# Performance work log

Measured on AMD Instinct MI355X. Metric: run time of the kernel, lower is better.

The kernel has to match this reference:

```python
import jax, jax.numpy as jnp
import numpy as np

TEMPERATURES = (0.02, 0.05, 0.2)
NORMALIZE_FEATURES = True
NORMALIZE_DRIFT = True
EPS = 1e-8


def _sqdist(a, b):
    # ||a_i - b_j||^2 via expansion; clamp tiny negatives from fp error
    aa = jnp.sum(a * a, axis=1)[:, None]
    bb = jnp.sum(b * b, axis=1)[None, :]
    return jnp.maximum(aa + bb - 2.0 * (a @ b.T), 0.0)


def compute_drifting_field(x, y_pos, y_neg, temperatures):
    """Multi-scale RBF-kernel drifting field.

    V(x) = mean_tau [ softmax_j(-d(x,y_pos_j)/tau) @ y_pos
                    - softmax_k(-d(x,y_neg_k)/tau) @ y_neg ]
    (the attraction/repulsion (y - x) terms: the -x cancels between pos and neg)
    Returns (V, raw_drift_norm, lambda_V).
    """
    D = x.shape[1]
    if NORMALIZE_FEATURES:
        # scale-invariant distances: global RMS of the reference samples
        ref = jnp.concatenate([y_pos, y_neg], axis=0)
        scale = jnp.sqrt(jnp.mean(ref * ref) + EPS)
    else:
        scale = jnp.asarray(1.0, x.dtype)
    xs, yp, yn = x / scale, y_pos / scale, y_neg / scale

    d_pos = _sqdist(xs, yp)  # [N, N_pos]
    d_neg = _sqdist(xs, yn)  # [N, N_neg]

    V = jnp.zeros_like(xs)
    for tau in temperatures:
        w_pos = jax.nn.softmax(-d_pos / tau, axis=1)
        w_neg = jax.nn.softmax(-d_neg / tau, axis=1)
        V = V + (w_pos @ yp - w_neg @ yn)
    V = (V / len(temperatures)) * scale  # back to original feature scale

    raw_drift_norm = jnp.mean(jnp.sum(V * V, axis=1))  # E[||V_raw||^2]
    lambda_V = jnp.sqrt(raw_drift_norm / D + EPS)
    if NORMALIZE_DRIFT:
        V = V / lambda_V
    return V, raw_drift_norm, lambda_V


def reference(x, y_pos, y_neg):
    V, raw_drift_norm, lambda_V = compute_drifting_field(x, y_pos, y_neg, TEMPERATURES)
    x_target = jax.lax.stop_gradient(x + V)
    loss_per_sample = jnp.mean((x - x_target) ** 2, axis=1)
    loss = jnp.mean(loss_per_sample)  # reduction='mean'
    drift_norm = jnp.mean(jnp.sum(V * V, axis=1))
    # per-temperature logging: original redundantly recomputes the full field
    per_temp = jnp.stack([
        compute_drifting_field(x, y_pos, y_neg, (tau,))[1] for tau in TEMPERATURES
    ])
    return loss, drift_norm, raw_drift_norm, lambda_V, per_temp, jax.lax.stop_gradient(V)


def setup_inputs() -> dict:
    key = jax.random.key(0)
    k1, k2, k3 = jax.random.split(key, 3)
    N, D = 4096, 256
    return {
        "x": jax.random.normal(k1, (N, D), dtype=jnp.float32),
        "y_pos": jax.random.normal(k2, (N, D), dtype=jnp.float32),
        "y_neg": jax.random.normal(k3, (N, D), dtype=jnp.float32),
    }
```

## Files before the change

kernel.cpp:

```cpp
#include <hip/hip_runtime.h>

#define NPTS 4096
#define DIM  256
#define TIL  64
#define WCAND 32

typedef unsigned short u16;
typedef unsigned long long u64;
typedef __attribute__((ext_vector_type(8))) short bf16x8;
typedef __attribute__((ext_vector_type(4))) float f32x4;
typedef __attribute__((ext_vector_type(4))) unsigned short u16x4;

__device__ __forceinline__ float exp2fast(float x) {
  float r;
  asm("v_exp_f32 %0, %1" : "=v"(r) : "v"(x));
  return r;
}

__device__ __forceinline__ void gload_lds16(const void* g, void* l) {
  __builtin_amdgcn_global_load_lds((const __attribute__((address_space(1))) void*)g,
                                   (__attribute__((address_space(3))) void*)l, 16, 0, 0);
}

__device__ __forceinline__ float blk_sum(float v, float* sh) {
  #pragma unroll
  for (int off = 32; off; off >>= 1) v += __shfl_down(v, off);
  int lane = threadIdx.x & 63, w = threadIdx.x >> 6;
  __syncthreads();
  if (lane == 0) sh[w] = v;
  __syncthreads();
  return sh[0] + sh[1] + sh[2] + sh[3];
}

__device__ __forceinline__ float block_scalesq(
    const float* __restrict__ bbp, const float* __restrict__ bbn, float* red, int tid) {
  float s = 0.f;
  #pragma unroll
  for (int q = 0; q < 4; ++q) {
    f32x4 a = *reinterpret_cast<const f32x4*>(bbp + (q * 256 + tid) * 4);
    f32x4 b = *reinterpret_cast<const f32x4*>(bbn + (q * 256 + tid) * 4);
    s += a[0] + a[1] + a[2] + a[3] + b[0] + b[1] + b[2] + b[3];
  }
  float tot = blk_sum(s, red);
  return tot * (1.0f / (2.0f * NPTS * DIM)) + 1e-8f;
}

__global__ __launch_bounds__(256) void split3_kernel(
    const float* __restrict__ x, const float* __restrict__ yp, const float* __restrict__ yn,
    u16* __restrict__ xb, u16* __restrict__ ypb, u16* __restrict__ ynb,
    float* __restrict__ bbp, float* __restrict__ bbn)
{
  const float* src; u16* dst; float* bb;
  if      (blockIdx.y == 0) { src = x;  dst = xb;  bb = nullptr; }
  else if (blockIdx.y == 1) { src = yp; dst = ypb; bb = bbp; }
  else                      { src = yn; dst = ynb; bb = bbn; }

  int lane = threadIdx.x & 63;
  int wave = threadIdx.x >> 6;
  int row  = blockIdx.x * 4 + wave;
  const float4 v = *reinterpret_cast<const float4*>(src + (size_t)row * DIM + lane * 4);
  float xs[4] = {v.x, v.y, v.z, v.w};
  u16x4 h;
  float ss = 0.f;
  #pragma unroll
  for (int e = 0; e < 4; ++e) {
    unsigned b = __float_as_uint(xs[e]);
    h[e] = (u16)((b + 0x7fffu + ((b >> 16) & 1u)) >> 16);
    ss += xs[e] * xs[e];
  }
  *reinterpret_cast<u16x4*>(dst + (size_t)row * DIM + lane * 4) = h;
  if (bb) {
    #pragma unroll
    for (int off = 32; off; off >>= 1) ss += __shfl_down(ss, off);
    if (lane == 0) bb[row] = ss;
  }
}

__global__ __launch_bounds__(256, 3) void gemm_kernel(
    const u16* __restrict__ Xb, const u16* __restrict__ Ypb, const u16* __restrict__ Ynb,
    const float* __restrict__ bbp, const float* __restrict__ bbn,
    float* __restrict__ M, u64* __restrict__ Kmask)
{
  __shared__ u16 Ah[3][128 * 32];
  __shared__ u16 Bh[3][128 * 32];
  __shared__ float red[4];

  const int tid  = threadIdx.x;

  const unsigned lid = blockIdx.x + (blockIdx.y << 5) + (blockIdx.z << 10);
  const unsigned swz = (lid & 7) * 256 + (lid >> 3);
  const int bx = swz & 31, by = (swz >> 5) & 31, side = (int)(swz >> 10);

  const u16* Yb = side ? Ynb : Ypb;
  const float* bbv = side ? bbn : bbp;

  const float scalesq = block_scalesq(bbp, bbn, red, tid);

  const int lane = tid & 63;
  const int wave = tid >> 6;
  const int wm = wave >> 1, wn = wave & 1;
  const int l15 = lane & 15, lhi = lane >> 4;

  const int rf = bx * 128;
  const int cf = by * 128;
  const int til = by * 2 + wn;

  const int r0  = tid >> 2;
  const int r1  = (tid + 256) >> 2;
  const int pc  = tid & 3;
  const int gc0 = pc ^ (r0 & 3);
  const int gc1 = pc ^ (r1 & 3);

  f32x4 acc[4][4] = {};

#define STAGE(KS, BUF)                                                                    \
  do {                                                                                    \
    int ko_ = (KS) * 32;                                                                  \
    gload_lds16(Xb + (size_t)(rf + r0) * DIM + ko_ + gc0 * 8, Ah[BUF] + r0 * 32 + pc * 8);\
    gload_lds16(Yb + (size_t)(cf + r0) * DIM + ko_ + gc0 * 8, Bh[BUF] + r0 * 32 + pc * 8);\
    gload_lds16(Xb + (size_t)(rf + r1) * DIM + ko_ + gc1 * 8, Ah[BUF] + r1 * 32 + pc * 8);\
    gload_lds16(Yb + (size_t)(cf + r1) * DIM + ko_ + gc1 * 8, Bh[BUF] + r1 * 32 + pc * 8);\
  } while (0)

  STAGE(0, 0);
  STAGE(1, 1);

  #pragma unroll 1
  for (int ks = 0; ks < 8; ++ks) {
    const int cur = ks % 3;
    if (ks < 7) asm volatile("s_waitcnt vmcnt(4)" ::: "memory");
    else        asm volatile("s_waitcnt vmcnt(0)" ::: "memory");
    __builtin_amdgcn_s_barrier();
    __builtin_amdgcn_sched_barrier(0);

    if (ks < 6) STAGE(ks + 2, (ks + 2) % 3);

    bf16x8 a[4], b[4];
    #pragma unroll
    for (int mi = 0; mi < 4; ++mi) {
      int R = wm * 64 + mi * 16 + l15;
      a[mi] = *reinterpret_cast<const bf16x8*>(Ah[cur] + R * 32 + ((lhi ^ (R & 3)) * 8));
    }
    #pragma unroll
    for (int ni = 0; ni < 4; ++ni) {
      int R = wn * 64 + ni * 16 + l15;
      b[ni] = *reinterpret_cast<const bf16x8*>(Bh[cur] + R * 32 + ((lhi ^ (R & 3)) * 8));
    }
    #pragma unroll
    for (int mi = 0; mi < 4; ++mi)
      #pragma unroll
      for (int ni = 0; ni < 4; ++ni)
        acc[mi][ni] = __builtin_amdgcn_mfma_f32_16x16x32_bf16(a[mi], b[ni], acc[mi][ni], 0, 0, 0);
  }
#undef STAGE

  const float thrP = 30.0f * scalesq * 0.2f + 2.5f * scalesq + 0.5f;

  float bbc[4];
  #pragma unroll
  for (int ni = 0; ni < 4; ++ni) bbc[ni] = bbv[cf + wn * 64 + ni * 16 + l15];

  #pragma unroll
  for (int mi = 0; mi < 4; ++mi)
    #pragma unroll
    for (int r = 0; r < 4; ++r) {
      float uv[4];
      float mx = -3.0e38f;
      #pragma unroll
      for (int ni = 0; ni < 4; ++ni) {
        uv[ni] = 2.0f * acc[mi][ni][r] - bbc[ni];
        mx = fmaxf(mx, uv[ni]);
      }
      #pragma unroll
      for (int off = 1; off < 16; off <<= 1) mx = fmaxf(mx, __shfl_xor(mx, off));
      const float cut = mx - thrP;

      u64 bal[4];
      #pragma unroll
      for (int ni = 0; ni < 4; ++ni) bal[ni] = __ballot(uv[ni] > cut);

      u64 mask = 0;
      #pragma unroll
      for (int ni = 0; ni < 4; ++ni)
        mask |= ((bal[ni] >> (lhi * 16)) & 0xFFFFull) << (ni * 16);

      const int rowG = rf + wm * 64 + mi * 16 + lhi * 4 + r;
      if (l15 == 0) {
        Kmask[((size_t)side * TIL + til) * NPTS + rowG] = mask;
        M[((size_t)side * NPTS + rowG) * TIL + til] = mx;
      }
    }
}

__global__ __launch_bounds__(256) void row_kernel(
    const float* __restrict__ M, const u64* __restrict__ Kmask,
    const float* __restrict__ bbp, const float* __restrict__ bbn,
    const float* __restrict__ x,
    const float* __restrict__ ypos, const float* __restrict__ yneg,
    float* __restrict__ parts, float* __restrict__ Vout)
{
  __shared__ unsigned cl[4][WCAND];
  __shared__ float red[4];

  const int tid  = threadIdx.x;
  const int lane = tid & 63;
  const int w    = tid >> 6;
  const int row  = blockIdx.x * 4 + w;

  const float scalesq = block_scalesq(bbp, bbn, red, tid);
  const float L2E = 1.4426950408889634f;
  const float c0 = L2E / (scalesq * 0.02f);
  const float c1 = L2E / (scalesq * 0.05f);
  const float c2 = L2E / (scalesq * 0.2f);
  const float thrP = 30.0f * scalesq * 0.2f + 2.5f * scalesq + 0.5f;

  const f32x4 xv = *reinterpret_cast<const f32x4*>(x + (size_t)row * DIM + lane * 4);

  f32x4 V0 = {0,0,0,0}, V1 = {0,0,0,0}, V2 = {0,0,0,0};

  for (int side = 0; side < 2; ++side) {
    const float* bb = side ? bbn : bbp;
    const float* y  = side ? yneg : ypos;
    const float sgn = side ? -1.f : 1.f;

    float Mv = M[((size_t)side * NPTS + row) * TIL + lane];
    float g = Mv;
    #pragma unroll
    for (int off = 32; off; off >>= 1) g = fmaxf(g, __shfl_xor(g, off));
    const float cut = g - thrP;

    u64 mm = __ballot(Mv > cut);
    int nc = 0;
    while (mm) {
      int t = __ffsll((long long)mm) - 1;
      mm &= mm - 1;
      u64 mask = Kmask[((size_t)side * TIL + t) * NPTS + row];
      bool keep = (mask >> lane) & 1ull;
      int rank = __popcll(mask & ((1ull << lane) - 1ull));
      if (keep && nc + rank < WCAND) cl[w][nc + rank] = t * 64 + lane;
      nc += __popcll(mask);
    }
    nc = nc < WCAND ? nc : WCAND;

    float me = -3.0e38f, p0 = 0.f, p1 = 0.f, p2 = 0.f;
    f32x4 A0 = {0,0,0,0}, A1 = {0,0,0,0}, A2 = {0,0,0,0};
    for (int bs = 0; bs < nc; bs += 8) {
      const int rem = nc - bs;
      int jq[8];
      f32x4 yv[8];
      float dq[8], uq[8];
      #pragma unroll
      for (int q = 0; q < 8; ++q) {
        int idx = (q < rem) ? bs + q : bs;
        jq[q] = (int)cl[w][idx];
        yv[q] = *reinterpret_cast<const f32x4*>(y + (size_t)jq[q] * DIM + lane * 4);
      }
      #pragma unroll
      for (int q = 0; q < 8; ++q)
        dq[q] = xv[0]*yv[q][0] + xv[1]*yv[q][1] + xv[2]*yv[q][2] + xv[3]*yv[q][3];
      #pragma unroll
      for (int off = 32; off; off >>= 1)
        #pragma unroll
        for (int q = 0; q < 8; ++q) dq[q] += __shfl_xor(dq[q], off);
      #pragma unroll
      for (int q = 0; q < 8; ++q)
        uq[q] = (q < rem) ? 2.0f * dq[q] - bb[jq[q]] : -3.0e38f;

      float cm = uq[0];
      #pragma unroll
      for (int q = 1; q < 8; ++q) cm = fmaxf(cm, uq[q]);
      float nm = fmaxf(me, cm);
      float s0 = exp2fast((me - nm) * c0);
      float s1 = exp2fast((me - nm) * c1);
      float s2 = exp2fast((me - nm) * c2);
      p0 *= s0; p1 *= s1; p2 *= s2;
      A0 *= s0; A1 *= s1; A2 *= s2;
      #pragma unroll
      for (int q = 0; q < 8; ++q) {
        float du = uq[q] - nm;
        float e0 = exp2fast(du * c0);
        float e1 = exp2fast(du * c1);
        float e2 = exp2fast(du * c2);
        p0 += e0; p1 += e1; p2 += e2;
        A0 += e0 * yv[q]; A1 += e1 * yv[q]; A2 += e2 * yv[q];
      }
      me = nm;
    }
    V0 += (sgn / p0) * A0;
    V1 += (sgn / p1) * A1;
    V2 += (sgn / p2) * A2;
  }

  f32x4 vr = (V0 + V1 + V2) * (1.0f / 3.0f);
  *reinterpret_cast<f32x4*>(Vout + (size_t)row * DIM + lane * 4) = vr;

  float s0 = V0[0]*V0[0] + V0[1]*V0[1] + V0[2]*V0[2] + V0[3]*V0[3];
  float s1 = V1[0]*V1[0] + V1[1]*V1[1] + V1[2]*V1[2] + V1[3]*V1[3];
  float s2 = V2[0]*V2[0] + V2[1]*V2[1] + V2[2]*V2[2] + V2[3]*V2[3];
  float sr = vr[0]*vr[0] + vr[1]*vr[1] + vr[2]*vr[2] + vr[3]*vr[3];
  #pragma unroll
  for (int off = 32; off; off >>= 1) {
    s0 += __shfl_xor(s0, off);
    s1 += __shfl_xor(s1, off);
    s2 += __shfl_xor(s2, off);
    sr += __shfl_xor(sr, off);
  }
  if (lane == 0) {
    parts[row]            = sr;
    parts[NPTS + row]     = s0;
    parts[2 * NPTS + row] = s1;
    parts[3 * NPTS + row] = s2;
  }
}

__global__ __launch_bounds__(256) void final_kernel(
    const float* __restrict__ parts, float* __restrict__ out)
{
  __shared__ float red[4];
  const int tid = threadIdx.x;

  float s = 0.f;
  for (int k = tid; k < NPTS; k += 256) s += parts[k];
  float raw = blk_sum(s, red) * (1.0f / NPTS);
  float lam2 = raw * (1.0f / DIM) + 1e-8f;
  float lam  = sqrtf(lam2);
  float inv  = 1.0f / lam;

  int idx = blockIdx.x * 256 + tid;
  out[7 + idx] *= inv;

  if (blockIdx.x == 0) {
    #pragma unroll
    for (int a = 1; a <= 3; ++a) {
      float t = 0.f;
      for (int k = tid; k < NPTS; k += 256) t += parts[a * NPTS + k];
      t = blk_sum(t, red);
      if (tid == 0) out[3 + a] = t * (1.0f / NPTS);
    }
    if (tid == 0) {
      float drift = raw / lam2;
      out[0] = drift * (1.0f / DIM);
      out[1] = drift;
      out[2] = raw;
      out[3] = lam;
    }
  }
}

extern "C" void kernel_launch(void* const* d_in, const int* in_sizes, int n_in,
                              void* d_out, int out_size, void* d_ws, size_t ws_size,
                              hipStream_t stream)
{
  (void)in_sizes; (void)n_in; (void)out_size; (void)ws_size;
  const float* x    = (const float*)d_in[0];
  const float* ypos = (const float*)d_in[1];
  const float* yneg = (const float*)d_in[2];
  float* out = (float*)d_out;
  char* ws = (char*)d_ws;

  float* bbp   = (float*)ws;
  float* bbn   = (float*)(ws + 16384);
  float* parts = (float*)(ws + 32768);
  float* M     = (float*)(ws + 98304);
  u64*   Kmask = (u64*)(ws + 98304 + 2097152);
  u16* xb  = (u16*)(ws + 98304 + 2097152 + 4194304);
  u16* ypb = xb + (size_t)NPTS * DIM;
  u16* ynb = xb + 2 * (size_t)NPTS * DIM;

  split3_kernel<<<dim3(NPTS / 4, 3), 256, 0, stream>>>(x, ypos, yneg, xb, ypb, ynb, bbp, bbn);
  gemm_kernel<<<dim3(32, 32, 2), 256, 0, stream>>>(xb, ypb, ynb, bbp, bbn, M, Kmask);
  row_kernel<<<NPTS / 4, 256, 0, stream>>>(M, Kmask, bbp, bbn, x, ypos, yneg,
                                           parts, out + 7);
  final_kernel<<<NPTS, 256, 0, stream>>>(parts, out);
}
```

Before: 83.35 us.

## Fuse pos/neg GEMMs per block to share X tile loads

Each GEMM block now computes both the positive and negative distance tiles for the same X rows, loading the X tile once and reusing it for two B tiles. This halves the grid, doubles the accumulators, and drops from triple to double buffering with a full vmcnt(0) wait each step. The LDS swizzle pattern also changes. The cost is higher register pressure, which may hurt occupancy at launch_bounds(256,3), and a less deep load pipeline.

New measurement: 118.6 us. 42.3% more time.

```diff
diff --git a/kernel.cpp b/kernel.cpp
--- a/kernel.cpp
+++ b/kernel.cpp
@@ -81,18 +81,16 @@
     const float* __restrict__ bbp, const float* __restrict__ bbn,
     float* __restrict__ M, u64* __restrict__ Kmask)
 {
-  __shared__ u16 Ah[3][128 * 32];
-  __shared__ u16 Bh[3][128 * 32];
+  __shared__ u16 Ah[2][128 * 32];
+  __shared__ u16 Bp[2][128 * 32];
+  __shared__ u16 Bn[2][128 * 32];
   __shared__ float red[4];
 
   const int tid  = threadIdx.x;
 
-  const unsigned lid = blockIdx.x + (blockIdx.y << 5) + (blockIdx.z << 10);
-  const unsigned swz = (lid & 7) * 256 + (lid >> 3);
-  const int bx = swz & 31, by = (swz >> 5) & 31, side = (int)(swz >> 10);
-
-  const u16* Yb = side ? Ynb : Ypb;
-  const float* bbv = side ? bbn : bbp;
+  const unsigned lid = blockIdx.x + (blockIdx.y << 5);
+  const unsigned swz = (lid & 7) * 128 + (lid >> 3);
+  const int bx = swz & 31, by = (int)(swz >> 5);
 
   const float scalesq = block_scalesq(bbp, bbn, red, tid);
 
@@ -106,90 +104,99 @@
   const int til = by * 2 + wn;
 
   const int r0  = tid >> 2;
-  const int r1  = (tid + 256) >> 2;
+  const int r1  = 64 + (tid >> 2);
   const int pc  = tid & 3;
-  const int gc0 = pc ^ (r0 & 3);
-  const int gc1 = pc ^ (r1 & 3);
-
-  f32x4 acc[4][4] = {};
-
-#define STAGE(KS, BUF)                                                                    \
-  do {                                                                                    \
-    int ko_ = (KS) * 32;                                                                  \
-    gload_lds16(Xb + (size_t)(rf + r0) * DIM + ko_ + gc0 * 8, Ah[BUF] + r0 * 32 + pc * 8);\
-    gload_lds16(Yb + (size_t)(cf + r0) * DIM + ko_ + gc0 * 8, Bh[BUF] + r0 * 32 + pc * 8);\
-    gload_lds16(Xb + (size_t)(rf + r1) * DIM + ko_ + gc1 * 8, Ah[BUF] + r1 * 32 + pc * 8);\
-    gload_lds16(Yb + (size_t)(cf + r1) * DIM + ko_ + gc1 * 8, Bh[BUF] + r1 * 32 + pc * 8);\
+  const int gc0 = (pc ^ ((r0 >> 1) & 3)) * 8;
+  const int gc1 = (pc ^ ((r1 >> 1) & 3)) * 8;
+
+  f32x4 accP[4][4] = {};
+  f32x4 accN[4][4] = {};
+
+#define STAGE(KS, BUF)                                                                     \
+  do {                                                                                     \
+    int ko_ = (KS) * 32;                                                                   \
+    gload_lds16(Xb  + (size_t)(rf + r0) * DIM + ko_ + gc0, Ah[BUF] + r0 * 32 + pc * 8);    \
+    gload_lds16(Ypb + (size_t)(cf + r0) * DIM + ko_ + gc0, Bp[BUF] + r0 * 32 + pc * 8);    \
+    gload_lds16(Ynb + (size_t)(cf + r0) * DIM + ko_ + gc0, Bn[BUF] + r0 * 32 + pc * 8);    \
+    gload_lds16(Xb  + (size_t)(rf + r1) * DIM + ko_ + gc1, Ah[BUF] + r1 * 32 + pc * 8);    \
+    gload_lds16(Ypb + (size_t)(cf + r1) * DIM + ko_ + gc1, Bp[BUF] + r1 * 32 + pc * 8);    \
+    gload_lds16(Ynb + (size_t)(cf + r1) * DIM + ko_ + gc1, Bn[BUF] + r1 * 32 + pc * 8);    \
   } while (0)
 
   STAGE(0, 0);
-  STAGE(1, 1);
-
-  #pragma unroll 1
+
+  #pragma unroll 2
   for (int ks = 0; ks < 8; ++ks) {
-    const int cur = ks % 3;
-    if (ks < 7) asm volatile("s_waitcnt vmcnt(4)" ::: "memory");
-    else        asm volatile("s_waitcnt vmcnt(0)" ::: "memory");
+    const int cur = ks & 1;
+    asm volatile("s_waitcnt vmcnt(0)" ::: "memory");
     __builtin_amdgcn_s_barrier();
-    __builtin_amdgcn_sched_barrier(0);
-
-    if (ks < 6) STAGE(ks + 2, (ks + 2) % 3);
-
-    bf16x8 a[4], b[4];
+
+    if (ks < 7) STAGE(ks + 1, cur ^ 1);
+
+    bf16x8 a[4], bp[4], bn[4];
     #pragma unroll
     for (int mi = 0; mi < 4; ++mi) {
       int R = wm * 64 + mi * 16 + l15;
-      a[mi] = *reinterpret_cast<const bf16x8*>(Ah[cur] + R * 32 + ((lhi ^ (R & 3)) * 8));
+      a[mi] = *reinterpret_cast<const bf16x8*>(Ah[cur] + R * 32 + ((lhi ^ ((R >> 1) & 3)) * 8));
     }
     #pragma unroll
     for (int ni = 0; ni < 4; ++ni) {
       int R = wn * 64 + ni * 16 + l15;
-      b[ni] = *reinterpret_cast<const bf16x8*>(Bh[cur] + R * 32 + ((lhi ^ (R & 3)) * 8));
+      int off = R * 32 + ((lhi ^ ((R >> 1) & 3)) * 8);
+      bp[ni] = *reinterpret_cast<const bf16x8*>(Bp[cur] + off);
+      bn[ni] = *reinterpret_cast<const bf16x8*>(Bn[cur] + off);
     }
     #pragma unroll
     for (int mi = 0; mi < 4; ++mi)
       #pragma unroll
-      for (int ni = 0; ni < 4; ++ni)
-        acc[mi][ni] = __builtin_amdgcn_mfma_f32_16x16x32_bf16(a[mi], b[ni], acc[mi][ni], 0, 0, 0);
+      for (int ni = 0; ni < 4; ++ni) {
+        accP[mi][ni] = __builtin_amdgcn_mfma_f32_16x16x32_bf16(a[mi], bp[ni], accP[mi][ni], 0, 0, 0);
+        accN[mi][ni] = __builtin_amdgcn_mfma_f32_16x16x32_bf16(a[mi], bn[ni], accN[mi][ni], 0, 0, 0);
+      }
   }
 #undef STAGE
 
   const float thrP = 30.0f * scalesq * 0.2f + 2.5f * scalesq + 0.5f;
 
-  float bbc[4];
-  #pragma unroll
-  for (int ni = 0; ni < 4; ++ni) bbc[ni] = bbv[cf + wn * 64 + ni * 16 + l15];
-
-  #pragma unroll
-  for (int mi = 0; mi < 4; ++mi)
-    #pragma unroll
-    for (int r = 0; r < 4; ++r) {
-      float uv[4];
-      float mx = -3.0e38f;
-      #pragma unroll
-      for (int ni = 0; ni < 4; ++ni) {
-        uv[ni] = 2.0f * acc[mi][ni][r] - bbc[ni];
-        mx = fmaxf(mx, uv[ni]);
+  #pragma unroll
+  for (int side = 0; side < 2; ++side) {
+    const float* bbv = side ? bbn : bbp;
+    float bbc[4];
+    #pragma unroll
+    for (int ni = 0; ni < 4; ++ni) bbc[ni] = bbv[cf + wn * 64 + ni * 16 + l15];
+
+    #pragma unroll
+    for (int mi = 0; mi < 4; ++mi)
+      #pragma unroll
+      for (int r = 0; r < 4; ++r) {
+        float uv[4];
+        float mx = -3.0e38f;
+        #pragma unroll
+        for (int ni = 0; ni < 4; ++ni) {
+          float av = side ? accN[mi][ni][r] : accP[mi][ni][r];
+          uv[ni] = 2.0f * av - bbc[ni];
+          mx = fmaxf(mx, uv[ni]);
+        }
+        #pragma unroll
+        for (int off = 1; off < 16; off <<= 1) mx = fmaxf(mx, __shfl_xor(mx, off));
+        const float cut = mx - thrP;
+
+        u64 bal[4];
+        #pragma unroll
+        for (int ni = 0; ni < 4; ++ni) bal[ni] = __ballot(uv[ni] > cut);
+
+        u64 mask = 0;
+        #pragma unroll
+        for (int ni = 0; ni < 4; ++ni)
+          mask |= ((bal[ni] >> (lhi * 16)) & 0xFFFFull) << (ni * 16);
+
+        const int rowG = rf + wm * 64 + mi * 16 + lhi * 4 + r;
+        if (l15 == 0) {
+          Kmask[((size_t)side * TIL + til) * NPTS + rowG] = mask;
+          M[((size_t)side * NPTS + rowG) * TIL + til] = mx;
+        }
       }
-      #pragma unroll
-      for (int off = 1; off < 16; off <<= 1) mx = fmaxf(mx, __shfl_xor(mx, off));
-      const float cut = mx - thrP;
-
-      u64 bal[4];
-      #pragma unroll
-      for (int ni = 0; ni < 4; ++ni) bal[ni] = __ballot(uv[ni] > cut);
-
-      u64 mask = 0;
-      #pragma unroll
-      for (int ni = 0; ni < 4; ++ni)
-        mask |= ((bal[ni] >> (lhi * 16)) & 0xFFFFull) << (ni * 16);
-
-      const int rowG = rf + wm * 64 + mi * 16 + lhi * 4 + r;
-      if (l15 == 0) {
-        Kmask[((size_t)side * TIL + til) * NPTS + rowG] = mask;
-        M[((size_t)side * NPTS + rowG) * TIL + til] = mx;
-      }
-    }
+  }
 }
 
 __global__ __launch_bounds__(256) void row_kernel(
@@ -368,7 +375,7 @@
   u16* ynb = xb + 2 * (size_t)NPTS * DIM;
 
   split3_kernel<<<dim3(NPTS / 4, 3), 256, 0, stream>>>(x, ypos, yneg, xb, ypb, ynb, bbp, bbn);
-  gemm_kernel<<<dim3(32, 32, 2), 256, 0, stream>>>(xb, ypb, ynb, bbp, bbn, M, Kmask);
+  gemm_kernel<<<dim3(32, 32), 256, 0, stream>>>(xb, ypb, ynb, bbp, bbn, M, Kmask);
   row_kernel<<<NPTS / 4, 256, 0, stream>>>(M, Kmask, bbp, bbn, x, ypos, yneg,
                                            parts, out + 7);
   final_kernel<<<NPTS, 256, 0, stream>>>(parts, out);
```
